# Kernel tuning notes

Measured on AMD Instinct MI355X. Metric: run time of the kernel, lower is better.

## Reference

```python
import jax, jax.numpy as jnp
import numpy as np

T, B, V, L = 512, 32, 512, 128
NEG = -1e9  # safe -inf surrogate (keeps logaddexp gradients finite)


def setup_inputs() -> dict:
    key = jax.random.key(0)
    k1, k2, k3 = jax.random.split(key, 3)
    log_probs = jax.nn.log_softmax(
        jax.random.normal(k1, (T, B, V), dtype=jnp.float32), axis=-1)
    # ASG transition parameter (init ones in the module; use small noise for a
    # non-degenerate reference). transition[i, j] = score of j -> i.
    transition = 0.1 * jax.random.normal(k2, (V, V), dtype=jnp.float32)
    targets = jax.random.randint(k3, (B, L), 0, V)
    input_lengths = jnp.full((B,), T, dtype=jnp.int32)
    target_lengths = jnp.full((B,), L, dtype=jnp.int32)
    return {"log_probs": log_probs, "transition": transition,
            "targets": targets, "input_lengths": input_lengths,
            "target_lengths": target_lengths}


def _fcc(log_probs, transition, input_lengths):
    """Fully-connected criterion: log-partition over all label paths. [B]"""
    def step(alpha, lp_t):  # alpha, lp_t: [B, V]
        # alpha'[b, i] = lp_t[b, i] + logsumexp_j(alpha[b, j] + trans[i, j])
        alpha = lp_t + jax.nn.logsumexp(
            alpha[:, None, :] + transition[None, :, :], axis=2)
        return alpha, jax.nn.logsumexp(alpha, axis=1)

    a0 = log_probs[0]
    _, tail = jax.lax.scan(step, a0, log_probs[1:])
    scores = jnp.concatenate(
        [jax.nn.logsumexp(a0, axis=1)[None], tail], axis=0)  # [T, B]
    return scores[input_lengths - 1, jnp.arange(scores.shape[1])]


def _fac(log_probs, transition, targets, input_lengths, target_lengths):
    """Forced-alignment criterion: DP constrained to the target label seq. [B]"""
    Tt, Bb, _ = log_probs.shape
    Ll = targets.shape[1]
    trans_self = transition[targets, targets]                    # [B, L] stay
    trans_prev = transition[targets[:, 1:], targets[:, :-1]]     # [B, L-1] advance
    # emit[t, b, s] = log_probs[t, b, targets[b, s]]
    emit = jnp.take_along_axis(
        log_probs, jnp.broadcast_to(targets[None], (Tt, Bb, Ll)), axis=2)

    sel = (target_lengths - 1)[:, None]  # [B, 1]

    def final_of(beta):
        return jnp.take_along_axis(beta, sel, axis=1)[:, 0]

    beta0 = jnp.where(jnp.arange(Ll)[None, :] == 0, emit[0], NEG)  # [B, L]

    def step(beta, em_t):
        stay = beta + trans_self
        move = jnp.concatenate(
            [jnp.full((Bb, 1), NEG, beta.dtype),
             beta[:, :-1] + trans_prev], axis=1)
        beta = em_t + jnp.logaddexp(stay, move)
        return beta, final_of(beta)

    _, tail = jax.lax.scan(step, beta0, emit[1:])
    fins = jnp.concatenate([final_of(beta0)[None], tail], axis=0)  # [T, B]
    return fins[input_lengths - 1, jnp.arange(Bb)]


def reference(log_probs, transition, targets, input_lengths, target_lengths):
    # ASG loss (reduction='none'): FCC - FAC, shape [B]
    fcc = _fcc(log_probs, transition, input_lengths)
    fac = _fac(log_probs, transition, targets, input_lengths, target_lengths)
    return fcc - fac
```

## Files before the change

### kernel.cpp

```cpp
#include <hip/hip_runtime.h>
#include <stdint.h>

#define T_ 512
#define B_ 32
#define V_ 512
#define L_ 128
#define NEGF (-1000000000.0f)

#define SE_Q 69.0f
#define SU_Q 127.0f
#define LOGC 9.078313f

typedef int v4i __attribute__((ext_vector_type(4)));

template <int CTRL>
__device__ __forceinline__ int dppmov(int old_, int src) {
    return __builtin_amdgcn_update_dpp(old_, src, CTRL, 0xF, 0xF, false);
}
__device__ __forceinline__ float wave_max64(float x) {
    int xi = __float_as_int(x);
    x = fmaxf(x, __int_as_float(dppmov<0x111>(xi, xi))); xi = __float_as_int(x);
    x = fmaxf(x, __int_as_float(dppmov<0x112>(xi, xi))); xi = __float_as_int(x);
    x = fmaxf(x, __int_as_float(dppmov<0x114>(xi, xi))); xi = __float_as_int(x);
    x = fmaxf(x, __int_as_float(dppmov<0x118>(xi, xi))); xi = __float_as_int(x);
    x = fmaxf(x, __int_as_float(dppmov<0x142>(xi, xi))); xi = __float_as_int(x);
    x = fmaxf(x, __int_as_float(dppmov<0x143>(xi, xi)));
    return x;
}
__device__ __forceinline__ float wave_sum64(float x) {
    int xi = __float_as_int(x);
    x = x + __int_as_float(dppmov<0x111>(xi, xi)); xi = __float_as_int(x);
    x = x + __int_as_float(dppmov<0x112>(xi, xi)); xi = __float_as_int(x);
    x = x + __int_as_float(dppmov<0x114>(xi, xi)); xi = __float_as_int(x);
    x = x + __int_as_float(dppmov<0x118>(xi, xi)); xi = __float_as_int(x);
    x = x + __int_as_float(dppmov<0x142>(xi, xi)); xi = __float_as_int(x);
    x = x + __int_as_float(dppmov<0x143>(xi, xi));
    return x;
}
__device__ __forceinline__ unsigned fkey(float f) {
    unsigned u = __float_as_uint(f);
    return (u & 0x80000000u) ? ~u : (u | 0x80000000u);
}
__device__ __forceinline__ float funkey(unsigned k) {
    unsigned u = (k & 0x80000000u) ? (k ^ 0x80000000u) : ~k;
    return __uint_as_float(u);
}
__device__ __forceinline__ int sel4(v4i a, int r) {
    int x0 = (r & 1) ? a.y : a.x;
    int x1 = (r & 1) ? a.w : a.z;
    return (r & 2) ? x1 : x0;
}

__global__ void asg_prep(const float* __restrict__ trans, uint32_t* __restrict__ Et) {
    int o = blockIdx.x * blockDim.x + threadIdx.x;
    int d    = o & 3;
    int tid  = (o >> 2) & 511;
    int qreg = o >> 11;
    int tt = qreg >> 3, kt = qreg & 7;
    int w = tid >> 6, lane = tid & 63;
    int q = lane >> 4, n = lane & 15;
    int m  = 64 * w + 16 * tt + n;
    int k0 = 64 * kt + 16 * q + 4 * d;
    const float* tp = trans + (size_t)m * V_ + k0;
    uint32_t q0 = (uint32_t)fminf(127.0f, __expf(tp[0]) * SE_Q + 0.5f);
    uint32_t q1 = (uint32_t)fminf(127.0f, __expf(tp[1]) * SE_Q + 0.5f);
    uint32_t q2 = (uint32_t)fminf(127.0f, __expf(tp[2]) * SE_Q + 0.5f);
    uint32_t q3 = (uint32_t)fminf(127.0f, __expf(tp[3]) * SE_Q + 0.5f);
    Et[(size_t)o] = q0 | (q1 << 8) | (q2 << 16) | (q3 << 24);
}

__global__ __attribute__((amdgpu_flat_work_group_size(512, 512),
                          amdgpu_waves_per_eu(2, 2)))
void asg_main(
    const float* __restrict__ lp, const uint32_t* __restrict__ Et,
    const float* __restrict__ trans, const int* __restrict__ targets,
    const int* __restrict__ ilen, const int* __restrict__ tlen,
    float* __restrict__ fcc_ws, float* __restrict__ fac_ws)
{
    __shared__ float facb[256];
    __shared__ __align__(16) uint32_t u_lds[2][128];
    __shared__ __align__(16) float mw_lds[2][8];
    __shared__ unsigned mslotE;
    __shared__ float sumf;

    const int bb  = blockIdx.x;
    const int tid = threadIdx.x;

    if (bb < B_) {
        const int b    = bb;
        const int lane = tid & 63;
        const int w    = tid >> 6;
        const int q    = lane >> 4;
        const int n    = lane & 15;
        const int tt_o = n >> 2;
        const int rg_o = n & 3;
        const int i    = 64 * w + 16 * tt_o + 4 * q + rg_o;
        const int Tlen = ilen[b];

        uint4 er4[32];
        {
            const uint4* Eq = (const uint4*)Et;
            #pragma unroll
            for (int t8 = 0; t8 < 32; ++t8) er4[t8] = Eq[t8 * 512 + tid];
        }

        float lpv0 = lp[(size_t)b * V_ + i];
        float elp  = __expf(lpv0);
        float lpv  = lp[(size_t)(B_ * V_) + (size_t)b * V_ + i];
        float accf = 1.0f;
        float S    = 0.0f;
        if (tid == 0) { mslotE = 0u; sumf = 0.0f; }
        __syncthreads();

        for (int t = 1; t < Tlen; ++t) {
            const int bi = t & 1;
            float key = elp * accf;

            float mxw = wave_max64(key);
            float kmax_w = __int_as_float(
                __builtin_amdgcn_readlane(__float_as_int(mxw), 63));
            kmax_w = fmaxf(kmax_w, 1e-30f);
            float r127 = 127.0f * __builtin_amdgcn_rcpf(kmax_w);

            {
                uint32_t qu = (uint32_t)fminf(127.0f, fmaf(key, r127, 0.5f));
                int pv = (int)(qu << (8 * (i & 3)));
                pv |= dppmov<0xB1>(pv, pv);
                pv |= dppmov<0x4E>(pv, pv);
                if ((i & 3) == 0) u_lds[bi][i >> 2] = (uint32_t)pv;
            }
            if (lane == 63) mw_lds[bi][w] = kmax_w;
            float elp_n = __expf(lpv);
            __syncthreads();

            uint4 bf[8];
            #pragma unroll
            for (int kt = 0; kt < 8; ++kt)
                bf[kt] = *(const uint4*)((const char*)u_lds[bi] + 64 * kt + 16 * q);
            float4 mv0 = *(const float4*)&mw_lds[bi][0];
            float4 mv1 = *(const float4*)&mw_lds[bi][4];

            int tn = (t + 1 < Tlen) ? (t + 1) : t;
            float lpv_n = lp[(size_t)tn * (B_ * V_) + (size_t)b * V_ + i];

            float kg = fmaxf(fmaxf(fmaxf(mv0.x, mv0.y), fmaxf(mv0.z, mv0.w)),
                             fmaxf(fmaxf(mv1.x, mv1.y), fmaxf(mv1.z, mv1.w)));
            float rkg = __builtin_amdgcn_rcpf(kg);
            float s0 = mv0.x * rkg, s1 = mv0.y * rkg;
            float s2 = mv0.z * rkg, s3 = mv0.w * rkg;
            float s4 = mv1.x * rkg, s5 = mv1.y * rkg;
            float s6 = mv1.z * rkg, s7 = mv1.w * rkg;

            int p[8];
            {
                v4i z = {0, 0, 0, 0};
                #pragma unroll
                for (int kt = 0; kt < 8; ++kt) {
                    v4i bv = __builtin_bit_cast(v4i, bf[kt]);
                    v4i a0 = __builtin_amdgcn_mfma_i32_16x16x64_i8(
                                __builtin_bit_cast(v4i, er4[0 * 8 + kt]), bv, z, 0, 0, 0);
                    v4i a1 = __builtin_amdgcn_mfma_i32_16x16x64_i8(
                                __builtin_bit_cast(v4i, er4[1 * 8 + kt]), bv, z, 0, 0, 0);
                    v4i a2 = __builtin_amdgcn_mfma_i32_16x16x64_i8(
                                __builtin_bit_cast(v4i, er4[2 * 8 + kt]), bv, z, 0, 0, 0);
                    v4i a3 = __builtin_amdgcn_mfma_i32_16x16x64_i8(
                                __builtin_bit_cast(v4i, er4[3 * 8 + kt]), bv, z, 0, 0, 0);
                    int x0 = sel4(a0, rg_o), x1 = sel4(a1, rg_o);
                    int x2 = sel4(a2, rg_o), x3 = sel4(a3, rg_o);
                    int y0 = (tt_o & 1) ? x1 : x0;
                    int y1 = (tt_o & 1) ? x3 : x2;
                    p[kt] = (tt_o & 2) ? y1 : y0;
                }
            }

            float t0 = fmaf(s0, (float)p[0], s1 * (float)p[1]);
            float t1 = fmaf(s2, (float)p[2], s3 * (float)p[3]);
            float t2 = fmaf(s4, (float)p[4], s5 * (float)p[5]);
            float t3 = fmaf(s6, (float)p[6], s7 * (float)p[7]);
            accf = (t0 + t1) + (t2 + t3);

            S += __logf(kg) - LOGC;
            elp = elp_n;
            lpv = lpv_n;
        }

        float alpha = ((Tlen > 1) ? lpv : lpv0) + S + __logf(accf);
        {
            float mx = wave_max64(alpha);
            if (lane == 63) atomicMax(&mslotE, fkey(mx));
        }
        __syncthreads();
        float m2 = funkey(mslotE);
        {
            float sv = wave_sum64(__expf(alpha - m2));
            if (lane == 63) atomicAdd(&sumf, sv);
        }
        __syncthreads();
        if (tid == 0) fcc_ws[b] = m2 + __logf(sumf);
    } else {
        const int b = bb - B_;
        const int l = tid;
        const bool active = (l < L_);
        const int Tlen = ilen[b];
        const int Llen = tlen[b];

        const int tl  = active ? targets[b * L_ + l] : 0;
        const int tlm = (active && l > 0) ? targets[b * L_ + l - 1] : 0;
        const float ts = active ? trans[(size_t)tl * V_ + tl] : 0.0f;
        const float tp = (active && l > 0) ? trans[(size_t)tl * V_ + tlm] : 0.0f;

        float beta = (l == 0) ? lp[(size_t)b * V_ + tl] : NEGF;
        float em_next = active ? lp[(size_t)1 * (B_ * V_) + (size_t)b * V_ + tl] : 0.0f;

        for (int t = 1; t < Tlen; ++t) {
            float* buf = facb + (t & 1) * L_;
            if (active) buf[l] = beta;
            __syncthreads();
            float prev = (active && l > 0) ? buf[l - 1] : NEGF;
            float em = em_next;
            if (active && t + 1 < Tlen)
                em_next = lp[(size_t)(t + 1) * (B_ * V_) + (size_t)b * V_ + tl];
            if (active) {
                float st = beta + ts;
                float mv = prev + tp;
                float mx = fmaxf(st, mv);
                float mn = fminf(st, mv);
                beta = em + mx + log1pf(__expf(mn - mx));
            }
        }
        if (active && l == Llen - 1) fac_ws[b] = beta;
    }
}

__global__ void asg_combine(const float* __restrict__ fcc_ws,
                            const float* __restrict__ fac_ws,
                            float* __restrict__ out) {
    int i = threadIdx.x;
    if (i < B_) out[i] = fcc_ws[i] - fac_ws[i];
}

extern "C" void kernel_launch(void* const* d_in, const int* in_sizes, int n_in,
                              void* d_out, int out_size, void* d_ws, size_t ws_size,
                              hipStream_t stream) {
    const float* lp      = (const float*)d_in[0];
    const float* trans   = (const float*)d_in[1];
    const int*   targets = (const int*)d_in[2];
    const int*   ilen    = (const int*)d_in[3];
    const int*   tlen    = (const int*)d_in[4];
    float* out = (float*)d_out;

    uint32_t* Et     = (uint32_t*)d_ws;
    float*    fcc_ws = (float*)((char*)d_ws + 65536 * 4);
    float*    fac_ws = fcc_ws + B_;

    hipLaunchKernelGGL(asg_prep, dim3(256), dim3(256), 0, stream, trans, Et);
    hipLaunchKernelGGL(asg_main, dim3(2 * B_), dim3(512), 0, stream,
                       lp, Et, trans, targets, ilen, tlen, fcc_ws, fac_ws);
    hipLaunchKernelGGL(asg_combine, dim3(1), dim3(64), 0, stream, fcc_ws, fac_ws, out);
}
```

Measured before the change: 667.3 us.

## Keep full MFMA output per lane and interleave MFMA with per-kt combine

Changes the FCC state ownership so each lane holds four consecutive states taken from the full MFMA accumulator vector, instead of picking one element with sel4. Lanes with n<4 become owners and write a packed quantized dword directly, which drops the DPP byte-packing shuffles. The MFMA calls are software-pipelined with two sets of accumulators so the scaling FMAs for one kt overlap the next MFMA batch. Lanes with n>=4 now do redundant work, the 1e-30 clamp on the wave max is removed, and per-lane register pressure goes up.

```diff
diff --git a/kernel.cpp b/kernel.cpp
--- a/kernel.cpp
+++ b/kernel.cpp
@@ -45,10 +45,20 @@
     unsigned u = (k & 0x80000000u) ? (k ^ 0x80000000u) : ~k;
     return __uint_as_float(u);
 }
-__device__ __forceinline__ int sel4(v4i a, int r) {
-    int x0 = (r & 1) ? a.y : a.x;
-    int x1 = (r & 1) ? a.w : a.z;
-    return (r & 2) ? x1 : x0;
+__device__ __forceinline__ void combine4(v4i c0, v4i c1, v4i c2, v4i c3,
+                                         bool tb0, bool tb1, float s,
+                                         float& a0, float& a1,
+                                         float& a2, float& a3) {
+    int y0x = tb0 ? c1.x : c0.x, y0y = tb0 ? c1.y : c0.y;
+    int y0z = tb0 ? c1.z : c0.z, y0w = tb0 ? c1.w : c0.w;
+    int y1x = tb0 ? c3.x : c2.x, y1y = tb0 ? c3.y : c2.y;
+    int y1z = tb0 ? c3.z : c2.z, y1w = tb0 ? c3.w : c2.w;
+    int sx = tb1 ? y1x : y0x, sy = tb1 ? y1y : y0y;
+    int sz = tb1 ? y1z : y0z, sw = tb1 ? y1w : y0w;
+    a0 = fmaf(s, (float)sx, a0);
+    a1 = fmaf(s, (float)sy, a1);
+    a2 = fmaf(s, (float)sz, a2);
+    a3 = fmaf(s, (float)sw, a3);
 }
 
 __global__ void asg_prep(const float* __restrict__ trans, uint32_t* __restrict__ Et) {
@@ -92,9 +102,12 @@
         const int w    = tid >> 6;
         const int q    = lane >> 4;
         const int n    = lane & 15;
-        const int tt_o = n >> 2;
-        const int rg_o = n & 3;
-        const int i    = 64 * w + 16 * tt_o + 4 * q + rg_o;
+        const int tto  = n & 3;
+        const bool own = (n < 4);
+        const bool tb0 = (tto & 1) != 0;
+        const bool tb1 = (tto & 2) != 0;
+        const int i0   = 64 * w + 16 * tto + 4 * q;
+        const int udw  = 16 * w + 4 * tto + q;
         const int Tlen = ilen[b];
 
         uint4 er4[32];
@@ -104,44 +117,55 @@
             for (int t8 = 0; t8 < 32; ++t8) er4[t8] = Eq[t8 * 512 + tid];
         }
 
-        float lpv0 = lp[(size_t)b * V_ + i];
-        float elp  = __expf(lpv0);
-        float lpv  = lp[(size_t)(B_ * V_) + (size_t)b * V_ + i];
-        float accf = 1.0f;
-        float S    = 0.0f;
+        float4 lp0 = *(const float4*)&lp[(size_t)b * V_ + i0];
+        float elp0 = __expf(lp0.x), elp1 = __expf(lp0.y);
+        float elp2 = __expf(lp0.z), elp3 = __expf(lp0.w);
+        float4 lpv = *(const float4*)&lp[(size_t)(B_ * V_) + (size_t)b * V_ + i0];
+        float ac0 = 1.0f, ac1 = 1.0f, ac2 = 1.0f, ac3 = 1.0f;
+        float S = 0.0f;
         if (tid == 0) { mslotE = 0u; sumf = 0.0f; }
         __syncthreads();
 
         for (int t = 1; t < Tlen; ++t) {
             const int bi = t & 1;
-            float key = elp * accf;
-
-            float mxw = wave_max64(key);
-            float kmax_w = __int_as_float(
+            uint32_t* ub = &u_lds[bi][0];
+            float*    mb = &mw_lds[bi][0];
+
+            float k0 = elp0 * ac0, k1 = elp1 * ac1;
+            float k2 = elp2 * ac2, k3 = elp3 * ac3;
+            float km = fmaxf(fmaxf(k0, k1), fmaxf(k2, k3));
+            float mxw = wave_max64(km);
+            float kw = __int_as_float(
                 __builtin_amdgcn_readlane(__float_as_int(mxw), 63));
-            kmax_w = fmaxf(kmax_w, 1e-30f);
-            float r127 = 127.0f * __builtin_amdgcn_rcpf(kmax_w);
+            float r127 = 127.0f * __builtin_amdgcn_rcpf(kw);
 
             {
-                uint32_t qu = (uint32_t)fminf(127.0f, fmaf(key, r127, 0.5f));
-                int pv = (int)(qu << (8 * (i & 3)));
-                pv |= dppmov<0xB1>(pv, pv);
-                pv |= dppmov<0x4E>(pv, pv);
-                if ((i & 3) == 0) u_lds[bi][i >> 2] = (uint32_t)pv;
+                uint32_t u0 = (uint32_t)fminf(127.0f, fmaf(k0, r127, 0.5f));
+                uint32_t u1 = (uint32_t)fminf(127.0f, fmaf(k1, r127, 0.5f));
+                uint32_t u2 = (uint32_t)fminf(127.0f, fmaf(k2, r127, 0.5f));
+                uint32_t u3 = (uint32_t)fminf(127.0f, fmaf(k3, r127, 0.5f));
+                uint32_t pack = u0 | (u1 << 8) | (u2 << 16) | (u3 << 24);
+                if (own) ub[udw] = pack;
             }
-            if (lane == 63) mw_lds[bi][w] = kmax_w;
-            float elp_n = __expf(lpv);
+            if (lane == 63) mb[w] = kw;
+
+            float elpn0 = __expf(lpv.x), elpn1 = __expf(lpv.y);
+            float elpn2 = __expf(lpv.z), elpn3 = __expf(lpv.w);
             __syncthreads();
 
-            uint4 bf[8];
-            #pragma unroll
-            for (int kt = 0; kt < 8; ++kt)
-                bf[kt] = *(const uint4*)((const char*)u_lds[bi] + 64 * kt + 16 * q);
-            float4 mv0 = *(const float4*)&mw_lds[bi][0];
-            float4 mv1 = *(const float4*)&mw_lds[bi][4];
+            uint4 bf0 = *(const uint4*)((const char*)ub +   0 + 16 * q);
+            uint4 bf1 = *(const uint4*)((const char*)ub +  64 + 16 * q);
+            uint4 bf2 = *(const uint4*)((const char*)ub + 128 + 16 * q);
+            uint4 bf3 = *(const uint4*)((const char*)ub + 192 + 16 * q);
+            uint4 bf4 = *(const uint4*)((const char*)ub + 256 + 16 * q);
+            uint4 bf5 = *(const uint4*)((const char*)ub + 320 + 16 * q);
+            uint4 bf6 = *(const uint4*)((const char*)ub + 384 + 16 * q);
+            uint4 bf7 = *(const uint4*)((const char*)ub + 448 + 16 * q);
+            float4 mv0 = *(const float4*)&mb[0];
+            float4 mv1 = *(const float4*)&mb[4];
 
             int tn = (t + 1 < Tlen) ? (t + 1) : t;
-            float lpv_n = lp[(size_t)tn * (B_ * V_) + (size_t)b * V_ + i];
+            float4 lvn = *(const float4*)&lp[(size_t)tn * (B_ * V_) + (size_t)b * V_ + i0];
 
             float kg = fmaxf(fmaxf(fmaxf(mv0.x, mv0.y), fmaxf(mv0.z, mv0.w)),
                              fmaxf(fmaxf(mv1.x, mv1.y), fmaxf(mv1.z, mv1.w)));
@@ -151,48 +175,59 @@
             float s4 = mv1.x * rkg, s5 = mv1.y * rkg;
             float s6 = mv1.z * rkg, s7 = mv1.w * rkg;
 
-            int p[8];
-            {
-                v4i z = {0, 0, 0, 0};
-                #pragma unroll
-                for (int kt = 0; kt < 8; ++kt) {
-                    v4i bv = __builtin_bit_cast(v4i, bf[kt]);
-                    v4i a0 = __builtin_amdgcn_mfma_i32_16x16x64_i8(
-                                __builtin_bit_cast(v4i, er4[0 * 8 + kt]), bv, z, 0, 0, 0);
-                    v4i a1 = __builtin_amdgcn_mfma_i32_16x16x64_i8(
-                                __builtin_bit_cast(v4i, er4[1 * 8 + kt]), bv, z, 0, 0, 0);
-                    v4i a2 = __builtin_amdgcn_mfma_i32_16x16x64_i8(
-                                __builtin_bit_cast(v4i, er4[2 * 8 + kt]), bv, z, 0, 0, 0);
-                    v4i a3 = __builtin_amdgcn_mfma_i32_16x16x64_i8(
-                                __builtin_bit_cast(v4i, er4[3 * 8 + kt]), bv, z, 0, 0, 0);
-                    int x0 = sel4(a0, rg_o), x1 = sel4(a1, rg_o);
-                    int x2 = sel4(a2, rg_o), x3 = sel4(a3, rg_o);
-                    int y0 = (tt_o & 1) ? x1 : x0;
-                    int y1 = (tt_o & 1) ? x3 : x2;
-                    p[kt] = (tt_o & 2) ? y1 : y0;
-                }
+            ac0 = 0.0f; ac1 = 0.0f; ac2 = 0.0f; ac3 = 0.0f;
+            v4i z = {0, 0, 0, 0};
+            v4i pA0, pA1, pA2, pA3, pB0, pB1, pB2, pB3;
+#define MFMA4(BF, KT, D0, D1, D2, D3)                                         \
+            {                                                                 \
+                v4i bv = __builtin_bit_cast(v4i, BF);                         \
+                D0 = __builtin_amdgcn_mfma_i32_16x16x64_i8(                   \
+                        __builtin_bit_cast(v4i, er4[0 * 8 + KT]), bv, z, 0, 0, 0); \
+                D1 = __builtin_amdgcn_mfma_i32_16x16x64_i8(                   \
+                        __builtin_bit_cast(v4i, er4[1 * 8 + KT]), bv, z, 0, 0, 0); \
+                D2 = __builtin_amdgcn_mfma_i32_16x16x64_i8(                   \
+                        __builtin_bit_cast(v4i, er4[2 * 8 + KT]), bv, z, 0, 0, 0); \
+                D3 = __builtin_amdgcn_mfma_i32_16x16x64_i8(                   \
+                        __builtin_bit_cast(v4i, er4[3 * 8 + KT]), bv, z, 0, 0, 0); \
             }
-
-            float t0 = fmaf(s0, (float)p[0], s1 * (float)p[1]);
-            float t1 = fmaf(s2, (float)p[2], s3 * (float)p[3]);
-            float t2 = fmaf(s4, (float)p[4], s5 * (float)p[5]);
-            float t3 = fmaf(s6, (float)p[6], s7 * (float)p[7]);
-            accf = (t0 + t1) + (t2 + t3);
+            MFMA4(bf0, 0, pA0, pA1, pA2, pA3);
+            MFMA4(bf1, 1, pB0, pB1, pB2, pB3);
+            combine4(pA0, pA1, pA2, pA3, tb0, tb1, s0, ac0, ac1, ac2, ac3);
+            MFMA4(bf2, 2, pA0, pA1, pA2, pA3);
+            combine4(pB0, pB1, pB2, pB3, tb0, tb1, s1, ac0, ac1, ac2, ac3);
+            MFMA4(bf3, 3, pB0, pB1, pB2, pB3);
+            combine4(pA0, pA1, pA2, pA3, tb0, tb1, s2, ac0, ac1, ac2, ac3);
+            MFMA4(bf4, 4, pA0, pA1, pA2, pA3);
+            combine4(pB0, pB1, pB2, pB3, tb0, tb1, s3, ac0, ac1, ac2, ac3);
+            MFMA4(bf5, 5, pB0, pB1, pB2, pB3);
+            combine4(pA0, pA1, pA2, pA3, tb0, tb1, s4, ac0, ac1, ac2, ac3);
+            MFMA4(bf6, 6, pA0, pA1, pA2, pA3);
+            combine4(pB0, pB1, pB2, pB3, tb0, tb1, s5, ac0, ac1, ac2, ac3);
+            MFMA4(bf7, 7, pB0, pB1, pB2, pB3);
+            combine4(pA0, pA1, pA2, pA3, tb0, tb1, s6, ac0, ac1, ac2, ac3);
+            combine4(pB0, pB1, pB2, pB3, tb0, tb1, s7, ac0, ac1, ac2, ac3);
+#undef MFMA4
 
             S += __logf(kg) - LOGC;
-            elp = elp_n;
-            lpv = lpv_n;
-        }
-
-        float alpha = ((Tlen > 1) ? lpv : lpv0) + S + __logf(accf);
+            elp0 = elpn0; elp1 = elpn1; elp2 = elpn2; elp3 = elpn3;
+            lpv = lvn;
+        }
+
+        float4 lpf = (Tlen > 1) ? lpv : lp0;
+        float al0 = lpf.x + S + __logf(ac0);
+        float al1 = lpf.y + S + __logf(ac1);
+        float al2 = lpf.z + S + __logf(ac2);
+        float al3 = lpf.w + S + __logf(ac3);
         {
-            float mx = wave_max64(alpha);
+            float mx = wave_max64(fmaxf(fmaxf(al0, al1), fmaxf(al2, al3)));
             if (lane == 63) atomicMax(&mslotE, fkey(mx));
         }
         __syncthreads();
         float m2 = funkey(mslotE);
         {
-            float sv = wave_sum64(__expf(alpha - m2));
+            float sv = own ? (__expf(al0 - m2) + __expf(al1 - m2) +
+                              __expf(al2 - m2) + __expf(al3 - m2)) : 0.0f;
+            sv = wave_sum64(sv);
             if (lane == 63) atomicAdd(&sumf, sv);
         }
         __syncthreads();
```

New measurement: 726.8 us. 1.09x slower.
